# Performance work log

Hardware: AMD Instinct MI355X
Metric: run time of the kernel (lower is better)

The kernel has to match this reference:

```python
import jax, jax.numpy as jnp
import numpy as np

SEQ, BATCH, IN, HID = 512, 64, 1024, 1024

def setup_inputs() -> dict:
    key = jax.random.key(0)
    k1, k2, k3 = jax.random.split(key, 3)
    X = jax.random.normal(k1, (SEQ, BATCH, IN), dtype=jnp.float32)
    hidden_state = jnp.zeros((BATCH, HID), dtype=jnp.float32)
    # nn.Linear(in, out, bias=False) weight has shape [out, in]
    W = jax.random.normal(k2, (HID, IN), dtype=jnp.float32) / np.sqrt(IN)
    H = jax.random.normal(k3, (HID, HID), dtype=jnp.float32) / np.sqrt(HID)
    return {"X": X, "hidden_state": hidden_state, "W": W, "H": H}

def reference(X, hidden_state, W, H):
    # Faithful to the torch code: hidden_state is NEVER updated inside the loop
    # (the module uses `hidden_state`, not `out`, each step), so
    #   out_t = tanh(X_t @ W^T + hidden_state @ H^T)   for every t,
    # and the H-term is constant across time. This vectorizes exactly.
    h_term = hidden_state @ H.T                      # [B, HID]
    output = jnp.tanh(jnp.einsum('tbi,hi->tbh', X, W) + h_term[None, :, :])  # [T,B,HID]
    return (output, output[-1])
```

## Files before the change

kernel.cpp:

```cpp
#include <hip/hip_runtime.h>


typedef __bf16 bf16x8 __attribute__((ext_vector_type(8)));
typedef float f32x4 __attribute__((ext_vector_type(4)));
typedef unsigned short us4 __attribute__((ext_vector_type(4)));

constexpr int M_TOT = 32768;
constexpr int K_D = 1024;
constexpr int N_D = 1024;
constexpr int BM = 256, BN = 128, BKT = 32;

__device__ __forceinline__ void async16(const void* g, void* l) {
  __builtin_amdgcn_global_load_lds(
      (const __attribute__((address_space(1))) unsigned int*)g,
      (__attribute__((address_space(3))) unsigned int*)l, 16, 0, 0);
}

__device__ __forceinline__ unsigned short f2bf(float f) {
  unsigned int u = __float_as_uint(f);
  u += 0x7FFFu + ((u >> 16) & 1u);
  return (unsigned short)(u >> 16);
}

constexpr int PREP_XBLK = M_TOT * K_D / 4 / 256;
constexpr int PREP_WBLK = N_D * K_D / 4 / 256;
constexpr int PREP_HBLK = 1024;
constexpr int PREP_GRID = PREP_XBLK + PREP_WBLK + PREP_HBLK;

__global__ __launch_bounds__(256) void prep_kernel(
    const float* __restrict__ X, unsigned short* __restrict__ Xbf,
    const float* __restrict__ W, unsigned short* __restrict__ Wbf,
    const float* __restrict__ hs, const float* __restrict__ Hm,
    float* __restrict__ ht) {
  __shared__ float4 Hrow4[256];
  const int b = blockIdx.x;
  const int tid = threadIdx.x;

  if (b < PREP_XBLK + PREP_WBLK) {
    const float* in = (b < PREP_XBLK) ? X : W;
    unsigned short* out = (b < PREP_XBLK) ? Xbf : Wbf;
    int j = (b < PREP_XBLK) ? (b * 256 + tid) : ((b - PREP_XBLK) * 256 + tid);
    int slot = j >> 1, half = j & 1;
    int row = slot >> 7, st = slot & 127;
    int sd = (st & ~3) | ((st & 3) ^ ((row >> 1) & 3));
    float4 a = *reinterpret_cast<const float4*>(in + (size_t)j * 4);
    us4 v;
    v[0] = f2bf(a.x); v[1] = f2bf(a.y); v[2] = f2bf(a.z); v[3] = f2bf(a.w);
    *reinterpret_cast<us4*>(out + (size_t)row * 1024 + sd * 8 + half * 4) = v;
  } else {
    int h = b - (PREP_XBLK + PREP_WBLK);
    Hrow4[tid] = reinterpret_cast<const float4*>(Hm + (size_t)h * 1024)[tid];
    __syncthreads();
    int w = tid >> 6, l = tid & 63;
#pragma unroll 2
    for (int bb = w * 16; bb < w * 16 + 16; ++bb) {
      const float4* hb4 = reinterpret_cast<const float4*>(hs + (size_t)bb * 1024);
      float s = 0.f;
#pragma unroll
      for (int p = 0; p < 4; ++p) {
        float4 x = hb4[l + p * 64];
        float4 y = Hrow4[l + p * 64];
        s += x.x * y.x + x.y * y.y + x.z * y.z + x.w * y.w;
      }
#pragma unroll
      for (int off = 32; off > 0; off >>= 1) s += __shfl_down(s, off, 64);
      if (l == 0) ht[bb * 1024 + h] = s;
    }
  }
}

__global__ __launch_bounds__(512, 4) void gemm_tanh(
    const unsigned short* __restrict__ A, const unsigned short* __restrict__ B,
    const float* __restrict__ ht, float* __restrict__ out0,
    float* __restrict__ out1) {
  __shared__ unsigned short As[BM * BKT];
  __shared__ unsigned short Bs[BN * BKT];

  int bid = blockIdx.x;
  int swz = (bid & 7) * 128 + (bid >> 3);
  int bm = swz >> 3;
  int bn = swz & 7;

  int tid = threadIdx.x;
  int lane = tid & 63, wid = tid >> 6;
  int wr = wid >> 1, wc = wid & 1;
  int fr = lane & 15, kq = lane >> 4;

  int c1 = tid + 512;
  const unsigned short* gA0 =
      A + (size_t)(bm * BM + (tid >> 2)) * 1024 + (tid & 3) * 8;
  const unsigned short* gA1 =
      A + (size_t)(bm * BM + (c1 >> 2)) * 1024 + (tid & 3) * 8;
  const unsigned short* gB0 =
      B + (size_t)(bn * BN + (tid >> 2)) * 1024 + (tid & 3) * 8;

  f32x4 acc[4][4] = {};

  for (int ks = 0; ks < K_D; ks += BKT) {
    async16(gA0 + ks, &As[tid * 8]);
    async16(gA1 + ks, &As[c1 * 8]);
    async16(gB0 + ks, &Bs[tid * 8]);
    __syncthreads();

    bf16x8 af[4], bg[4];
#pragma unroll
    for (int mi = 0; mi < 4; ++mi) {
      int ra = wr * 64 + mi * 16 + fr;
      af[mi] = *reinterpret_cast<const bf16x8*>(
          &As[ra * BKT + (kq ^ ((ra >> 1) & 3)) * 8]);
    }
#pragma unroll
    for (int ni = 0; ni < 4; ++ni) {
      int rb = wc * 64 + ni * 16 + fr;
      bg[ni] = *reinterpret_cast<const bf16x8*>(
          &Bs[rb * BKT + (kq ^ ((rb >> 1) & 3)) * 8]);
    }
#pragma unroll
    for (int mi = 0; mi < 4; ++mi)
#pragma unroll
      for (int ni = 0; ni < 4; ++ni)
        acc[mi][ni] = __builtin_amdgcn_mfma_f32_16x16x32_bf16(
            af[mi], bg[ni], acc[mi][ni], 0, 0, 0);
    __syncthreads();
  }

  const int nbase = bn * BN + wc * 64;
#pragma unroll
  for (int mi = 0; mi < 4; ++mi) {
#pragma unroll
    for (int r = 0; r < 4; ++r) {
      int mloc = wr * 64 + mi * 16 + kq * 4 + r;
      size_t m = (size_t)bm * BM + mloc;
      int b = mloc & 63;
#pragma unroll
      for (int ni = 0; ni < 4; ++ni) {
        int n = nbase + ni * 16 + fr;
        float x = acc[mi][ni][r] + ht[b * 1024 + n];
        float e = __expf(2.0f * x);
        float y = 1.0f - 2.0f / (e + 1.0f);
        out0[m * 1024 + n] = y;
        if (m >= (size_t)(M_TOT - 64))
          out1[(m - (M_TOT - 64)) * 1024 + n] = y;
      }
    }
  }
}

extern "C" void kernel_launch(void* const* d_in, const int* in_sizes, int n_in,
                              void* d_out, int out_size, void* d_ws,
                              size_t ws_size, hipStream_t stream) {
  (void)in_sizes; (void)n_in; (void)out_size; (void)ws_size;
  const float* X  = (const float*)d_in[0];
  const float* hs = (const float*)d_in[1];
  const float* W  = (const float*)d_in[2];
  const float* Hm = (const float*)d_in[3];
  float* out0 = (float*)d_out;
  float* out1 = out0 + (size_t)M_TOT * N_D;

  unsigned short* Xbf = (unsigned short*)d_ws;
  unsigned short* Wbf = Xbf + (size_t)M_TOT * K_D;
  float* hterm = (float*)(Wbf + (size_t)N_D * K_D);

  prep_kernel<<<PREP_GRID, 256, 0, stream>>>(X, Xbf, W, Wbf, hs, Hm, hterm);
  gemm_tanh<<<(M_TOT / BM) * (N_D / BN), 512, 0, stream>>>(Xbf, Wbf, hterm,
                                                           out0, out1);
}
```

Measured before the change: 157.1 us.

## Fuse X fp32-to-bf16 conversion into GEMM and retile to 64x512

```diff
diff --git a/kernel.cpp b/kernel.cpp
--- a/kernel.cpp
+++ b/kernel.cpp
@@ -8,7 +8,7 @@
 constexpr int M_TOT = 32768;
 constexpr int K_D = 1024;
 constexpr int N_D = 1024;
-constexpr int BM = 256, BN = 128, BKT = 32;
+constexpr int BM = 64, BN = 512, BKT = 32;
 
 __device__ __forceinline__ void async16(const void* g, void* l) {
   __builtin_amdgcn_global_load_lds(
@@ -22,13 +22,11 @@
   return (unsigned short)(u >> 16);
 }
 
-constexpr int PREP_XBLK = M_TOT * K_D / 4 / 256;
 constexpr int PREP_WBLK = N_D * K_D / 4 / 256;
 constexpr int PREP_HBLK = 1024;
-constexpr int PREP_GRID = PREP_XBLK + PREP_WBLK + PREP_HBLK;
+constexpr int PREP_GRID = PREP_WBLK + PREP_HBLK;
 
 __global__ __launch_bounds__(256) void prep_kernel(
-    const float* __restrict__ X, unsigned short* __restrict__ Xbf,
     const float* __restrict__ W, unsigned short* __restrict__ Wbf,
     const float* __restrict__ hs, const float* __restrict__ Hm,
     float* __restrict__ ht) {
@@ -36,19 +34,17 @@
   const int b = blockIdx.x;
   const int tid = threadIdx.x;
 
-  if (b < PREP_XBLK + PREP_WBLK) {
-    const float* in = (b < PREP_XBLK) ? X : W;
-    unsigned short* out = (b < PREP_XBLK) ? Xbf : Wbf;
-    int j = (b < PREP_XBLK) ? (b * 256 + tid) : ((b - PREP_XBLK) * 256 + tid);
+  if (b < PREP_WBLK) {
+    int j = b * 256 + tid;
     int slot = j >> 1, half = j & 1;
     int row = slot >> 7, st = slot & 127;
     int sd = (st & ~3) | ((st & 3) ^ ((row >> 1) & 3));
-    float4 a = *reinterpret_cast<const float4*>(in + (size_t)j * 4);
+    float4 a = *reinterpret_cast<const float4*>(W + (size_t)j * 4);
     us4 v;
     v[0] = f2bf(a.x); v[1] = f2bf(a.y); v[2] = f2bf(a.z); v[3] = f2bf(a.w);
-    *reinterpret_cast<us4*>(out + (size_t)row * 1024 + sd * 8 + half * 4) = v;
+    *reinterpret_cast<us4*>(Wbf + (size_t)row * 1024 + sd * 8 + half * 4) = v;
   } else {
-    int h = b - (PREP_XBLK + PREP_WBLK);
+    int h = b - PREP_WBLK;
     Hrow4[tid] = reinterpret_cast<const float4*>(Hm + (size_t)h * 1024)[tid];
     __syncthreads();
     int w = tid >> 6, l = tid & 63;
@@ -69,51 +65,57 @@
   }
 }
 
-__global__ __launch_bounds__(512, 4) void gemm_tanh(
-    const unsigned short* __restrict__ A, const unsigned short* __restrict__ B,
+__global__ __launch_bounds__(512, 4) void gemm_fused(
+    const float* __restrict__ X, const unsigned short* __restrict__ B,
     const float* __restrict__ ht, float* __restrict__ out0,
     float* __restrict__ out1) {
+  __shared__ unsigned short Bs[BN * BKT];
   __shared__ unsigned short As[BM * BKT];
-  __shared__ unsigned short Bs[BN * BKT];
 
   int bid = blockIdx.x;
-  int swz = (bid & 7) * 128 + (bid >> 3);
-  int bm = swz >> 3;
-  int bn = swz & 7;
+  int idx = bid >> 3;
+  int bm = (bid & 7) * 64 + (idx >> 1);
+  int bn = idx & 1;
 
   int tid = threadIdx.x;
   int lane = tid & 63, wid = tid >> 6;
-  int wr = wid >> 1, wc = wid & 1;
   int fr = lane & 15, kq = lane >> 4;
 
-  int c1 = tid + 512;
-  const unsigned short* gA0 =
-      A + (size_t)(bm * BM + (tid >> 2)) * 1024 + (tid & 3) * 8;
-  const unsigned short* gA1 =
-      A + (size_t)(bm * BM + (c1 >> 2)) * 1024 + (tid & 3) * 8;
-  const unsigned short* gB0 =
-      B + (size_t)(bn * BN + (tid >> 2)) * 1024 + (tid & 3) * 8;
+  const unsigned short* gB[4];
+#pragma unroll
+  for (int i = 0; i < 4; ++i) {
+    int c = tid + i * 512;
+    gB[i] = B + (size_t)(bn * BN + (c >> 2)) * 1024 + (c & 3) * 8;
+  }
+  const float* gX = X + (size_t)(bm * BM + (tid >> 3)) * 1024 + (tid & 7) * 4;
+  const int awr = tid >> 3;
+  const int aws = ((tid & 7) >> 1) ^ ((awr >> 1) & 3);
+  unsigned short* aw = &As[awr * 32 + aws * 8 + (tid & 1) * 4];
 
   f32x4 acc[4][4] = {};
 
   for (int ks = 0; ks < K_D; ks += BKT) {
-    async16(gA0 + ks, &As[tid * 8]);
-    async16(gA1 + ks, &As[c1 * 8]);
-    async16(gB0 + ks, &Bs[tid * 8]);
+    float4 a4 = *reinterpret_cast<const float4*>(gX + ks);
+#pragma unroll
+    for (int i = 0; i < 4; ++i)
+      async16(gB[i] + ks, &Bs[(tid + i * 512) * 8]);
+    us4 v;
+    v[0] = f2bf(a4.x); v[1] = f2bf(a4.y); v[2] = f2bf(a4.z); v[3] = f2bf(a4.w);
+    *reinterpret_cast<us4*>(aw) = v;
     __syncthreads();
 
     bf16x8 af[4], bg[4];
 #pragma unroll
     for (int mi = 0; mi < 4; ++mi) {
-      int ra = wr * 64 + mi * 16 + fr;
+      int ra = mi * 16 + fr;
       af[mi] = *reinterpret_cast<const bf16x8*>(
-          &As[ra * BKT + (kq ^ ((ra >> 1) & 3)) * 8]);
+          &As[ra * 32 + (kq ^ ((ra >> 1) & 3)) * 8]);
     }
 #pragma unroll
     for (int ni = 0; ni < 4; ++ni) {
-      int rb = wc * 64 + ni * 16 + fr;
+      int rb = wid * 64 + ni * 16 + fr;
       bg[ni] = *reinterpret_cast<const bf16x8*>(
-          &Bs[rb * BKT + (kq ^ ((rb >> 1) & 3)) * 8]);
+          &Bs[rb * 32 + (kq ^ ((rb >> 1) & 3)) * 8]);
     }
 #pragma unroll
     for (int mi = 0; mi < 4; ++mi)
@@ -124,14 +126,14 @@
     __syncthreads();
   }
 
-  const int nbase = bn * BN + wc * 64;
+  const int nbase = bn * BN + wid * 64;
 #pragma unroll
   for (int mi = 0; mi < 4; ++mi) {
 #pragma unroll
     for (int r = 0; r < 4; ++r) {
-      int mloc = wr * 64 + mi * 16 + kq * 4 + r;
+      int mloc = mi * 16 + kq * 4 + r;
       size_t m = (size_t)bm * BM + mloc;
-      int b = mloc & 63;
+      int b = mloc;
 #pragma unroll
       for (int ni = 0; ni < 4; ++ni) {
         int n = nbase + ni * 16 + fr;
@@ -157,11 +159,10 @@
   float* out0 = (float*)d_out;
   float* out1 = out0 + (size_t)M_TOT * N_D;
 
-  unsigned short* Xbf = (unsigned short*)d_ws;
-  unsigned short* Wbf = Xbf + (size_t)M_TOT * K_D;
+  unsigned short* Wbf = (unsigned short*)d_ws;
   float* hterm = (float*)(Wbf + (size_t)N_D * K_D);
 
-  prep_kernel<<<PREP_GRID, 256, 0, stream>>>(X, Xbf, W, Wbf, hs, Hm, hterm);
-  gemm_tanh<<<(M_TOT / BM) * (N_D / BN), 512, 0, stream>>>(Xbf, Wbf, hterm,
-                                                           out0, out1);
+  prep_kernel<<<PREP_GRID, 256, 0, stream>>>(W, Wbf, hs, Hm, hterm);
+  gemm_fused<<<(M_TOT / BM) * (N_D / BN), 512, 0, stream>>>(X, Wbf, hterm,
+                                                            out0, out1);
 }
```

Result: slower. 191.9 us (+22.1%).

## Triple-buffer LDS tiles with async prefetch two stages ahead in GEMM

Applied to the files above, without the earlier changes.

```diff
diff --git a/kernel.cpp b/kernel.cpp
--- a/kernel.cpp
+++ b/kernel.cpp
@@ -9,6 +9,9 @@
 constexpr int K_D = 1024;
 constexpr int N_D = 1024;
 constexpr int BM = 256, BN = 128, BKT = 32;
+constexpr int NTK = K_D / BKT;
+constexpr int ATILE = BM * BKT;
+constexpr int BTILE = BN * BKT;
 
 __device__ __forceinline__ void async16(const void* g, void* l) {
   __builtin_amdgcn_global_load_lds(
@@ -73,8 +76,8 @@
     const unsigned short* __restrict__ A, const unsigned short* __restrict__ B,
     const float* __restrict__ ht, float* __restrict__ out0,
     float* __restrict__ out1) {
-  __shared__ unsigned short As[BM * BKT];
-  __shared__ unsigned short Bs[BN * BKT];
+  __shared__ unsigned short As[3][ATILE];
+  __shared__ unsigned short Bs[3][BTILE];
 
   int bid = blockIdx.x;
   int swz = (bid & 7) * 128 + (bid >> 3);
@@ -96,32 +99,53 @@
 
   f32x4 acc[4][4] = {};
 
-  for (int ks = 0; ks < K_D; ks += BKT) {
-    async16(gA0 + ks, &As[tid * 8]);
-    async16(gA1 + ks, &As[c1 * 8]);
-    async16(gB0 + ks, &Bs[tid * 8]);
-    __syncthreads();
+#define STAGE(kt, buf)                                  \
+  {                                                     \
+    async16(gA0 + (kt) * BKT, &As[buf][tid * 8]);       \
+    async16(gA1 + (kt) * BKT, &As[buf][c1 * 8]);        \
+    async16(gB0 + (kt) * BKT, &Bs[buf][tid * 8]);       \
+  }
+
+  STAGE(0, 0);
+  STAGE(1, 1);
+  asm volatile("s_waitcnt vmcnt(3)" ::: "memory");
+  __builtin_amdgcn_s_barrier();
+  asm volatile("" ::: "memory");
+
+  for (int kt = 0; kt < NTK; ++kt) {
+    const int cur = kt % 3;
+    if (kt + 2 < NTK) STAGE(kt + 2, (kt + 2) % 3);
 
     bf16x8 af[4], bg[4];
 #pragma unroll
     for (int mi = 0; mi < 4; ++mi) {
       int ra = wr * 64 + mi * 16 + fr;
       af[mi] = *reinterpret_cast<const bf16x8*>(
-          &As[ra * BKT + (kq ^ ((ra >> 1) & 3)) * 8]);
+          &As[cur][ra * BKT + (kq ^ ((ra >> 1) & 3)) * 8]);
     }
 #pragma unroll
     for (int ni = 0; ni < 4; ++ni) {
       int rb = wc * 64 + ni * 16 + fr;
       bg[ni] = *reinterpret_cast<const bf16x8*>(
-          &Bs[rb * BKT + (kq ^ ((rb >> 1) & 3)) * 8]);
+          &Bs[cur][rb * BKT + (kq ^ ((rb >> 1) & 3)) * 8]);
     }
+    __builtin_amdgcn_s_setprio(1);
 #pragma unroll
     for (int mi = 0; mi < 4; ++mi)
 #pragma unroll
       for (int ni = 0; ni < 4; ++ni)
         acc[mi][ni] = __builtin_amdgcn_mfma_f32_16x16x32_bf16(
             af[mi], bg[ni], acc[mi][ni], 0, 0, 0);
-    __syncthreads();
+    __builtin_amdgcn_s_setprio(0);
+
+    if (kt + 1 < NTK) {
+      if (kt + 2 < NTK)
+        asm volatile("s_waitcnt vmcnt(3)" ::: "memory");
+      else
+        asm volatile("s_waitcnt vmcnt(0)" ::: "memory");
+      __builtin_amdgcn_s_barrier();
+      asm volatile("" ::: "memory");
+    }
   }
 
   const int nbase = bn * BN + wc * 64;
@@ -144,6 +168,7 @@
       }
     }
   }
+#undef STAGE
 }
 
 extern "C" void kernel_launch(void* const* d_in, const int* in_sizes, int n_in,
```

Result: no change. 155.7 us (-0.9%).

## Rewrite GEMM mainloop as 256x256x64 tile with double-buffered async LDS pipeline

Applied to the files above, without the earlier changes.

```diff
diff --git a/kernel.cpp b/kernel.cpp
--- a/kernel.cpp
+++ b/kernel.cpp
@@ -8,7 +8,10 @@
 constexpr int M_TOT = 32768;
 constexpr int K_D = 1024;
 constexpr int N_D = 1024;
-constexpr int BM = 256, BN = 128, BKT = 32;
+constexpr int BM = 256, BN = 256, BK = 64;
+constexpr int NKT = K_D / BK;
+constexpr int NIT = NKT / 2;
+constexpr int HALF = 128 * 64;
 
 __device__ __forceinline__ void async16(const void* g, void* l) {
   __builtin_amdgcn_global_load_lds(
@@ -42,7 +45,7 @@
     int j = (b < PREP_XBLK) ? (b * 256 + tid) : ((b - PREP_XBLK) * 256 + tid);
     int slot = j >> 1, half = j & 1;
     int row = slot >> 7, st = slot & 127;
-    int sd = (st & ~3) | ((st & 3) ^ ((row >> 1) & 3));
+    int sd = (st & ~7) | ((st & 7) ^ (row & 7));
     float4 a = *reinterpret_cast<const float4*>(in + (size_t)j * 4);
     us4 v;
     v[0] = f2bf(a.x); v[1] = f2bf(a.y); v[2] = f2bf(a.z); v[3] = f2bf(a.w);
@@ -69,68 +72,152 @@
   }
 }
 
-__global__ __launch_bounds__(512, 4) void gemm_tanh(
+__global__ __launch_bounds__(512, 2) void gemm_tanh(
     const unsigned short* __restrict__ A, const unsigned short* __restrict__ B,
     const float* __restrict__ ht, float* __restrict__ out0,
     float* __restrict__ out1) {
-  __shared__ unsigned short As[BM * BKT];
-  __shared__ unsigned short Bs[BN * BKT];
+  __shared__ unsigned short As[2][2][HALF];
+  __shared__ unsigned short Bs[2][2][HALF];
 
   int bid = blockIdx.x;
-  int swz = (bid & 7) * 128 + (bid >> 3);
-  int bm = swz >> 3;
-  int bn = swz & 7;
+  int swz = (bid & 7) * 64 + (bid >> 3);
+  int bm = swz >> 2;
+  int bn = swz & 3;
 
   int tid = threadIdx.x;
   int lane = tid & 63, wid = tid >> 6;
-  int wr = wid >> 1, wc = wid & 1;
+  int wr = wid >> 2, wc = wid & 3;
   int fr = lane & 15, kq = lane >> 4;
 
-  int c1 = tid + 512;
-  const unsigned short* gA0 =
-      A + (size_t)(bm * BM + (tid >> 2)) * 1024 + (tid & 3) * 8;
-  const unsigned short* gA1 =
-      A + (size_t)(bm * BM + (c1 >> 2)) * 1024 + (tid & 3) * 8;
-  const unsigned short* gB0 =
-      B + (size_t)(bn * BN + (tid >> 2)) * 1024 + (tid & 3) * 8;
-
-  f32x4 acc[4][4] = {};
-
-  for (int ks = 0; ks < K_D; ks += BKT) {
-    async16(gA0 + ks, &As[tid * 8]);
-    async16(gA1 + ks, &As[c1 * 8]);
-    async16(gB0 + ks, &Bs[tid * 8]);
-    __syncthreads();
-
-    bf16x8 af[4], bg[4];
-#pragma unroll
-    for (int mi = 0; mi < 4; ++mi) {
-      int ra = wr * 64 + mi * 16 + fr;
-      af[mi] = *reinterpret_cast<const bf16x8*>(
-          &As[ra * BKT + (kq ^ ((ra >> 1) & 3)) * 8]);
-    }
-#pragma unroll
-    for (int ni = 0; ni < 4; ++ni) {
-      int rb = wc * 64 + ni * 16 + fr;
-      bg[ni] = *reinterpret_cast<const bf16x8*>(
-          &Bs[rb * BKT + (kq ^ ((rb >> 1) & 3)) * 8]);
-    }
-#pragma unroll
-    for (int mi = 0; mi < 4; ++mi)
-#pragma unroll
-      for (int ni = 0; ni < 4; ++ni)
-        acc[mi][ni] = __builtin_amdgcn_mfma_f32_16x16x32_bf16(
-            af[mi], bg[ni], acc[mi][ni], 0, 0, 0);
-    __syncthreads();
-  }
-
-  const int nbase = bn * BN + wc * 64;
-#pragma unroll
-  for (int mi = 0; mi < 4; ++mi) {
+  const int arow = bm * BM;
+  const int brow = bn * BN;
+
+  f32x4 acc[8][4] = {};
+  bf16x8 bg[4][2];
+
+#define STG(g_, rowbase_, ks_, lds_)                                       \
+  {                                                                        \
+    _Pragma("unroll") for (int i_ = 0; i_ < 2; ++i_) {                     \
+      int c_ = tid + i_ * 512;                                             \
+      async16((g_) + (size_t)((rowbase_) + (c_ >> 3)) * 1024 + (ks_) +     \
+                  (c_ & 7) * 8,                                            \
+              (lds_) + c_ * 8);                                            \
+    }                                                                      \
+  }
+
+#define LOAD_BG(bi_)                                                       \
+  {                                                                        \
+    _Pragma("unroll") for (int ni_ = 0; ni_ < 4; ++ni_)                    \
+        _Pragma("unroll") for (int kk_ = 0; kk_ < 2; ++kk_) {              \
+      int rb_ = (wc & 1) * 64 + ni_ * 16 + fr;                             \
+      bg[ni_][kk_] = *reinterpret_cast<const bf16x8*>(                     \
+          &Bs[bi_][wc >> 1][rb_ * 64 + ((kk_ * 4 + kq) ^ (rb_ & 7)) * 8]); \
+    }                                                                      \
+  }
+
+#define LOAD_AF(bi_, q_)                                                   \
+  {                                                                        \
+    _Pragma("unroll") for (int dm_ = 0; dm_ < 2; ++dm_)                    \
+        _Pragma("unroll") for (int kk_ = 0; kk_ < 2; ++kk_) {              \
+      int ra_ = ((q_) * 2 + dm_) * 16 + fr;                                \
+      af[dm_][kk_] = *reinterpret_cast<const bf16x8*>(                     \
+          &As[bi_][wr][ra_ * 64 + ((kk_ * 4 + kq) ^ (ra_ & 7)) * 8]);      \
+    }                                                                      \
+  }
+
+#define MFMA_Q(q_)                                                         \
+  {                                                                        \
+    __builtin_amdgcn_s_setprio(1);                                         \
+    _Pragma("unroll") for (int dm_ = 0; dm_ < 2; ++dm_)                    \
+        _Pragma("unroll") for (int ni_ = 0; ni_ < 4; ++ni_)                \
+            _Pragma("unroll") for (int kk_ = 0; kk_ < 2; ++kk_)            \
+                acc[(q_) * 2 + dm_][ni_] =                                 \
+        __builtin_amdgcn_mfma_f32_16x16x32_bf16(                           \
+            af[dm_][kk_], bg[ni_][kk_], acc[(q_) * 2 + dm_][ni_], 0, 0, 0);\
+    __builtin_amdgcn_s_setprio(0);                                         \
+  }
+
+#define BAR() __builtin_amdgcn_s_barrier()
+
+  STG(A, arow + 0,   0, &As[0][0][0]);
+  STG(A, arow + 128, 0, &As[0][1][0]);
+  STG(B, brow + 0,   0, &Bs[0][0][0]);
+  STG(B, brow + 128, 0, &Bs[0][1][0]);
+  STG(B, brow + 0,   BK, &Bs[1][0][0]);
+  STG(B, brow + 128, BK, &Bs[1][1][0]);
+  asm volatile("s_waitcnt vmcnt(4)" ::: "memory");
+  BAR();
+
+  for (int j = 0; j < NIT; ++j) {
+    const int kt1 = 2 * j + 1;
+    const int kn = 2 * j + 2;
+    const bool nl = (j < NIT - 1);
+
+    {
+      bf16x8 af[2][2];
+      LOAD_BG(0); LOAD_AF(0, 0);
+      STG(A, arow + 0, kt1 * BK, &As[1][0][0]);
+      BAR(); MFMA_Q(0); BAR();
+    }
+    {
+      bf16x8 af[2][2];
+      LOAD_AF(0, 1);
+      STG(A, arow + 128, kt1 * BK, &As[1][1][0]);
+      BAR(); MFMA_Q(1); BAR();
+    }
+    {
+      bf16x8 af[2][2];
+      LOAD_AF(0, 2);
+      if (nl) STG(B, brow + 0, kn * BK, &Bs[0][0][0]);
+      BAR(); MFMA_Q(2); BAR();
+    }
+    {
+      bf16x8 af[2][2];
+      LOAD_AF(0, 3);
+      if (nl) STG(B, brow + 128, kn * BK, &Bs[0][1][0]);
+      BAR(); MFMA_Q(3);
+      if (nl)
+        asm volatile("s_waitcnt vmcnt(4)" ::: "memory");
+      else
+        asm volatile("s_waitcnt vmcnt(0)" ::: "memory");
+      BAR();
+    }
+    {
+      bf16x8 af[2][2];
+      LOAD_BG(1); LOAD_AF(1, 0);
+      if (nl) STG(A, arow + 0, kn * BK, &As[0][0][0]);
+      BAR(); MFMA_Q(0); BAR();
+    }
+    {
+      bf16x8 af[2][2];
+      LOAD_AF(1, 1);
+      if (nl) STG(A, arow + 128, kn * BK, &As[0][1][0]);
+      BAR(); MFMA_Q(1); BAR();
+    }
+    {
+      bf16x8 af[2][2];
+      LOAD_AF(1, 2);
+      if (nl) STG(B, brow + 0, (kn + 1) * BK, &Bs[1][0][0]);
+      BAR(); MFMA_Q(2); BAR();
+    }
+    {
+      bf16x8 af[2][2];
+      LOAD_AF(1, 3);
+      if (nl) STG(B, brow + 128, (kn + 1) * BK, &Bs[1][1][0]);
+      BAR(); MFMA_Q(3);
+      if (nl) asm volatile("s_waitcnt vmcnt(4)" ::: "memory");
+      BAR();
+    }
+  }
+
+  const int nbase = brow + wc * 64;
+  const int mbase = arow + wr * 128;
+#pragma unroll
+  for (int mi = 0; mi < 8; ++mi) {
 #pragma unroll
     for (int r = 0; r < 4; ++r) {
-      int mloc = wr * 64 + mi * 16 + kq * 4 + r;
-      size_t m = (size_t)bm * BM + mloc;
+      int mloc = mi * 16 + kq * 4 + r;
+      size_t m = (size_t)mbase + mloc;
       int b = mloc & 63;
 #pragma unroll
       for (int ni = 0; ni < 4; ++ni) {
@@ -144,6 +231,11 @@
       }
     }
   }
+#undef STG
+#undef LOAD_BG
+#undef LOAD_AF
+#undef MFMA_Q
+#undef BAR
 }
 
 extern "C" void kernel_launch(void* const* d_in, const int* in_sizes, int n_in,
```

Measured after the change: 180.5 us. +14.9%, slower.
